# Optimization experiments

Measured on AMD Instinct MI355X. Metric: run time of the kernel, lower is better.

The kernel has to match this reference:

```python
import jax, jax.numpy as jnp
import numpy as np

N, E = 50000, 800000
NODE_DIM, EDGE_DIM, HID = 128, 32, 128
NEG_SLOPE = 0.2


def _init(key, shape, fan_in):
    # glorot-ish init for weights
    return jax.random.normal(key, shape, dtype=jnp.float32) * (1.0 / np.sqrt(fan_in))


def setup_inputs() -> dict:
    key = jax.random.key(0)
    ks = jax.random.split(key, 20)
    x = jax.random.normal(ks[0], (N, NODE_DIM), dtype=jnp.float32)
    edge_index = jax.random.randint(ks[1], (2, E), 0, N, dtype=jnp.int64)
    edge_attr = jax.random.normal(ks[2], (E, EDGE_DIM), dtype=jnp.float32)
    params = {
        'W_emb': _init(ks[3], (NODE_DIM, HID), NODE_DIM),
        'b_emb': jnp.zeros((HID,), jnp.float32),
        # conv1 (GATv2Conv, heads=1)
        'Wl1': _init(ks[4], (HID, HID), HID), 'bl1': jnp.zeros((HID,), jnp.float32),
        'Wr1': _init(ks[5], (HID, HID), HID),
        'We1': _init(ks[6], (EDGE_DIM, HID), EDGE_DIM),
        'att1': _init(ks[7], (HID,), HID),
        'bo1': jnp.zeros((HID,), jnp.float32),
        # conv2
        'Wl2': _init(ks[8], (HID, HID), HID), 'bl2': jnp.zeros((HID,), jnp.float32),
        'Wr2': _init(ks[9], (HID, HID), HID),
        'We2': _init(ks[10], (EDGE_DIM, HID), EDGE_DIM),
        'att2': _init(ks[11], (HID,), HID),
        'bo2': jnp.zeros((HID,), jnp.float32),
    }
    return {'x': x, 'edge_index': edge_index, 'edge_attr': edge_attr, **params}


def _gatv2(x, src, dst, edge_attr, Wl, bl, Wr, We, att, bo, n_nodes):
    """PyG GATv2Conv (heads=1, add_self_loops=True, fill_value='mean')."""
    xl = x @ Wl + bl          # [N, H] source transform
    xr = x @ Wr               # [N, H] target transform
    # --- add self loops; self-loop edge_attr = mean of incoming edge_attr ---
    ones = jnp.ones((src.shape[0],), x.dtype)
    deg = jax.ops.segment_sum(ones, dst, num_segments=n_nodes)
    loop_attr = jax.ops.segment_sum(edge_attr, dst, num_segments=n_nodes) \
        / jnp.maximum(deg, 1.0)[:, None]
    loops = jnp.arange(n_nodes, dtype=src.dtype)
    src2 = jnp.concatenate([src, loops])
    dst2 = jnp.concatenate([dst, loops])
    ea2 = jnp.concatenate([edge_attr, loop_attr], axis=0)
    # --- per-edge attention (GATv2: leaky_relu AFTER the sum, score via att) ---
    xl_j = xl[src2]                                  # [E', H]
    msg = xl_j + xr[dst2] + ea2 @ We                 # [E', H]
    logits = jax.nn.leaky_relu(msg, NEG_SLOPE) @ att  # [E']
    # --- softmax over incoming edges per target node ---
    m = jax.ops.segment_max(logits, dst2, num_segments=n_nodes)
    ez = jnp.exp(logits - m[dst2])
    denom = jax.ops.segment_sum(ez, dst2, num_segments=n_nodes)
    alpha = ez / denom[dst2]                         # [E']
    # --- scatter-add aggregation ---
    out = jax.ops.segment_sum(alpha[:, None] * xl_j, dst2, num_segments=n_nodes)
    return out + bo


def reference(x, edge_index, edge_attr, W_emb, b_emb,
              Wl1, bl1, Wr1, We1, att1, bo1,
              Wl2, bl2, Wr2, We2, att2, bo2):
    src, dst = edge_index[0], edge_index[1]
    n = x.shape[0]
    h = x @ W_emb + b_emb
    h = jax.nn.silu(_gatv2(h, src, dst, edge_attr, Wl1, bl1, Wr1, We1, att1, bo1, n))
    h = jax.nn.silu(_gatv2(h, src, dst, edge_attr, Wl2, bl2, Wr2, We2, att2, bo2, n))
    return h
```

## Files before the change

### kernel.cpp

```cpp
#include <hip/hip_runtime.h>
#include <hip/hip_bf16.h>
#include <math.h>


#define HIP_N 50000
#define HIP_E 800000
#define HIP_H 128
#define HIP_ED 32
#define NEG_SLOPE 0.2f
#define RESCALE_THR_LOG2 11.5416f
#define LINB ((HIP_N + 31) / 32)
#define SCATB ((HIP_E + 255) / 256)
#define INV_LN2 1.4426950408889634f

typedef __fp16 h2 __attribute__((ext_vector_type(2)));

__device__ __forceinline__ h2 u2h(unsigned int u) {
    union { unsigned int u; h2 h; } c; c.u = u; return c.h;
}
__device__ __forceinline__ unsigned int pkh(float a, float b) {
    union { h2 h; unsigned int u; } c;
    c.h = __builtin_amdgcn_cvt_pkrtz(a, b);
    return c.u;
}
__device__ __forceinline__ float2 h2f(unsigned int u) {
    h2 h = u2h(u);
    return make_float2((float)h.x, (float)h.y);
}

__global__ void k_detect(const int* __restrict__ ei, int* __restrict__ is32) {
    int j = blockIdx.x * blockDim.x + threadIdx.x;
    if (j < 4096) {
        if (ei[2 * j + 1] != 0) atomicOr(is32, 1);
    }
}

__device__ __forceinline__ int fetch_idx(const int* __restrict__ ei, int is32, long long pos) {
    return is32 ? ei[pos] : ei[2 * pos];
}

__global__ void k_hist(const int* __restrict__ ei, const int* __restrict__ flag,
                       int* __restrict__ deg) {
    int is32 = *flag;
    int e = blockIdx.x * blockDim.x + threadIdx.x;
    if (e < HIP_E) {
        int d = fetch_idx(ei, is32, (long long)HIP_E + e);
        atomicAdd(&deg[d], 1);
    }
}

#define SCAN_TILE 1024
#define SCAN_NB ((HIP_N + SCAN_TILE - 1) / SCAN_TILE)

__global__ __launch_bounds__(256) void k_scan1(const int* __restrict__ deg,
                                               int* __restrict__ bsums) {
    __shared__ int ws[4];
    int b = blockIdx.x, t = threadIdx.x;
    int base = b * SCAN_TILE;
    int v = 0;
#pragma unroll
    for (int j = 0; j < 4; ++j) {
        int i = base + t + 256 * j;
        if (i < HIP_N) v += deg[i];
    }
#pragma unroll
    for (int off = 32; off > 0; off >>= 1) v += __shfl_xor(v, off);
    int lane = t & 63, wid = t >> 6;
    if (lane == 0) ws[wid] = v;
    __syncthreads();
    if (t == 0) bsums[b] = ws[0] + ws[1] + ws[2] + ws[3];
}

__global__ __launch_bounds__(64) void k_scan2(const int* __restrict__ bsums,
                                              int* __restrict__ bscan) {
    int t = threadIdx.x;
    int v = (t < SCAN_NB) ? bsums[t] : 0;
    int incl = v;
#pragma unroll
    for (int off = 1; off < 64; off <<= 1) {
        int u = __shfl_up(incl, off);
        if (t >= off) incl += u;
    }
    if (t < SCAN_NB) bscan[t] = incl - v;
}

__global__ __launch_bounds__(1024) void k_scan3(const int* __restrict__ deg,
                                                const int* __restrict__ bscan,
                                                int* __restrict__ offs,
                                                int* __restrict__ cursor) {
    __shared__ int wsum[16];
    int b = blockIdx.x, t = threadIdx.x;
    int i = b * SCAN_TILE + t;
    int lane = t & 63, wid = t >> 6;
    int v = (i < HIP_N) ? deg[i] : 0;
    int incl = v;
#pragma unroll
    for (int off = 1; off < 64; off <<= 1) {
        int u = __shfl_up(incl, off);
        if (lane >= off) incl += u;
    }
    if (lane == 63) wsum[wid] = incl;
    __syncthreads();
    if (wid == 0 && lane < 16) {
        int w = wsum[lane];
#pragma unroll
        for (int off = 1; off < 16; off <<= 1) {
            int u = __shfl_up(w, off);
            if (lane >= off) w += u;
        }
        wsum[lane] = w;
    }
    __syncthreads();
    int baseadd = bscan[b] + (wid > 0 ? wsum[wid - 1] : 0);
    int excl = baseadd + incl - v;
    if (i < HIP_N) {
        offs[i] = excl;
        cursor[i] = excl;
        if (i == HIP_N - 1) offs[HIP_N] = excl + v;
    }
}

__device__ __forceinline__ void lin_body(const float* __restrict__ h,
                                         const float* __restrict__ Wl,
                                         const float* __restrict__ bl,
                                         const float* __restrict__ Wr,
                                         const float* __restrict__ br,
                                         unsigned int* __restrict__ xlh,
                                         unsigned int* __restrict__ xrh,
                                         int n, int blk) {
    __shared__ float tile[32][128];
    int rb = blk * 32;
    int tid = threadIdx.x;
    for (int j = 0; j < 16; ++j) {
        int idx = j * 256 + tid;
        int r = idx >> 7, c = idx & 127;
        int row = rb + r;
        tile[r][c] = (row < n) ? h[(size_t)row * 128 + c] : 0.f;
    }
    __syncthreads();
    int c = tid & 127, g = tid >> 7;
    float accl[16], accr[16];
#pragma unroll
    for (int r = 0; r < 16; ++r) { accl[r] = 0.f; accr[r] = 0.f; }
    for (int d4 = 0; d4 < 32; ++d4) {
        int d = d4 * 4;
        float wl0 = Wl[(d + 0) * 128 + c];
        float wl1 = Wl[(d + 1) * 128 + c];
        float wl2 = Wl[(d + 2) * 128 + c];
        float wl3 = Wl[(d + 3) * 128 + c];
        float wr0 = Wr[(d + 0) * 128 + c];
        float wr1 = Wr[(d + 1) * 128 + c];
        float wr2 = Wr[(d + 2) * 128 + c];
        float wr3 = Wr[(d + 3) * 128 + c];
#pragma unroll
        for (int r = 0; r < 16; ++r) {
            const float4 hv = *(const float4*)&tile[g * 16 + r][d];
            accl[r] += hv.x * wl0 + hv.y * wl1 + hv.z * wl2 + hv.w * wl3;
            accr[r] += hv.x * wr0 + hv.y * wr1 + hv.z * wr2 + hv.w * wr3;
        }
    }
    float bbl = bl[c], bbr = br[c];
    bool evenc = !(c & 1);
#pragma unroll
    for (int r = 0; r < 16; ++r) {
        int row = rb + g * 16 + r;
        float vl = accl[r] + bbl;
        float vr = accr[r] + bbr;
        float vl1 = __shfl_down(vl, 1);
        float vr1 = __shfl_down(vr, 1);
        if (evenc && row < n) {
            xlh[(size_t)row * 64 + (c >> 1)] = pkh(vl, vl1);
            xrh[(size_t)row * 64 + (c >> 1)] = pkh(vr, vr1);
        }
    }
}

__device__ __forceinline__ void scatter_body(const int* __restrict__ ei, int is32,
                                             int* __restrict__ cursor,
                                             int* __restrict__ e_src,
                                             const float* __restrict__ ea,
                                             unsigned int* __restrict__ ea_h, int e) {
    if (e < HIP_E) {
        int s = fetch_idx(ei, is32, e);
        int d = fetch_idx(ei, is32, (long long)HIP_E + e);
        int pos = atomicAdd(&cursor[d], 1);
        e_src[pos] = s;
        const float4* src4 = (const float4*)(ea + (size_t)e * HIP_ED);
        float4 s0 = src4[0], s1 = src4[1], s2 = src4[2], s3 = src4[3];
        float4 s4 = src4[4], s5 = src4[5], s6 = src4[6], s7 = src4[7];
        uint4* dst = (uint4*)(ea_h + (size_t)pos * 16);
        dst[0] = make_uint4(pkh(s0.x, s0.y), pkh(s0.z, s0.w),
                            pkh(s1.x, s1.y), pkh(s1.z, s1.w));
        dst[1] = make_uint4(pkh(s2.x, s2.y), pkh(s2.z, s2.w),
                            pkh(s3.x, s3.y), pkh(s3.z, s3.w));
        dst[2] = make_uint4(pkh(s4.x, s4.y), pkh(s4.z, s4.w),
                            pkh(s5.x, s5.y), pkh(s5.z, s5.w));
        dst[3] = make_uint4(pkh(s6.x, s6.y), pkh(s6.z, s6.w),
                            pkh(s7.x, s7.y), pkh(s7.z, s7.w));
    }
}

__global__ __launch_bounds__(256) void k_fat1(
    const float* __restrict__ x, const float* __restrict__ Wl,
    const float* __restrict__ bl, const float* __restrict__ Wr,
    const float* __restrict__ br,
    unsigned int* __restrict__ xlh, unsigned int* __restrict__ xrh,
    const int* __restrict__ ei, const int* __restrict__ flag,
    int* __restrict__ cursor, int* __restrict__ e_src,
    const float* __restrict__ ea, unsigned int* __restrict__ ea_h) {
    if (blockIdx.x < LINB) {
        lin_body(x, Wl, bl, Wr, br, xlh, xrh, HIP_N, blockIdx.x);
    } else {
        int e = (blockIdx.x - LINB) * 256 + threadIdx.x;
        scatter_body(ei, *flag, cursor, e_src, ea, ea_h, e);
    }
}

__global__ __launch_bounds__(256) void k_lin(const float* __restrict__ h,
                                             const float* __restrict__ Wl,
                                             const float* __restrict__ bl,
                                             const float* __restrict__ Wr,
                                             const float* __restrict__ br,
                                             unsigned int* __restrict__ xlh,
                                             unsigned int* __restrict__ xrh, int n) {
    lin_body(h, Wl, bl, Wr, br, xlh, xrh, n, blockIdx.x);
}

__global__ __launch_bounds__(128) void k_compose(
    const float* __restrict__ Wemb, const float* __restrict__ bemb,
    const float* __restrict__ Wl, const float* __restrict__ bl,
    const float* __restrict__ Wr,
    float* __restrict__ Wlf, float* __restrict__ blf,
    float* __restrict__ Wrf, float* __restrict__ brf,
    float* __restrict__ zerob) {
    int b = blockIdx.x, c = threadIdx.x;
    if (b < 128) {
        float acc = 0.f;
        for (int k = 0; k < 128; ++k) acc += Wemb[b * 128 + k] * Wl[k * 128 + c];
        Wlf[b * 128 + c] = acc;
    } else if (b < 256) {
        int r = b - 128;
        float acc = 0.f;
        for (int k = 0; k < 128; ++k) acc += Wemb[r * 128 + k] * Wr[k * 128 + c];
        Wrf[r * 128 + c] = acc;
    } else if (b == 256) {
        float acc = bl[c];
        for (int k = 0; k < 128; ++k) acc += bemb[k] * Wl[k * 128 + c];
        blf[c] = acc;
    } else {
        float acc = 0.f;
        for (int k = 0; k < 128; ++k) acc += bemb[k] * Wr[k * 128 + c];
        brf[c] = acc;
        zerob[c] = 0.f;
    }
}

__global__ __launch_bounds__(256) void k_packwe(const float* __restrict__ We1,
                                                const float* __restrict__ We2,
                                                unsigned int* __restrict__ P1,
                                                unsigned int* __restrict__ P2) {
    int idx = blockIdx.x * 256 + threadIdx.x;
    if (idx < 4096) {
        const float* We = (idx < 2048) ? We1 : We2;
        unsigned int* P = (idx < 2048) ? P1 : P2;
        int r = idx & 2047;
        int d2 = r >> 7, rem = r & 127;
        int j = rem >> 6, t = rem & 63;
        int col = 2 * t + j;
        P[r] = pkh(We[(2 * d2) * 128 + col], We[(2 * d2 + 1) * 128 + col]);
    }
}

__global__ __launch_bounds__(64) void k_node_fused(
    const int* __restrict__ offs, const int* __restrict__ e_src,
    const unsigned int* __restrict__ ea_h,
    const unsigned int* __restrict__ Wepk, const float* __restrict__ att,
    const unsigned int* __restrict__ xlh, const unsigned int* __restrict__ xrh,
    const float* __restrict__ bo, float* __restrict__ hout) {
    int i = blockIdx.x;
    int t = threadIdx.x;

    h2 wx00 = u2h(Wepk[ 0*128 + t]),      wy00 = u2h(Wepk[ 0*128 + 64 + t]);
    h2 wx01 = u2h(Wepk[ 1*128 + t]),      wy01 = u2h(Wepk[ 1*128 + 64 + t]);
    h2 wx02 = u2h(Wepk[ 2*128 + t]),      wy02 = u2h(Wepk[ 2*128 + 64 + t]);
    h2 wx03 = u2h(Wepk[ 3*128 + t]),      wy03 = u2h(Wepk[ 3*128 + 64 + t]);
    h2 wx04 = u2h(Wepk[ 4*128 + t]),      wy04 = u2h(Wepk[ 4*128 + 64 + t]);
    h2 wx05 = u2h(Wepk[ 5*128 + t]),      wy05 = u2h(Wepk[ 5*128 + 64 + t]);
    h2 wx06 = u2h(Wepk[ 6*128 + t]),      wy06 = u2h(Wepk[ 6*128 + 64 + t]);
    h2 wx07 = u2h(Wepk[ 7*128 + t]),      wy07 = u2h(Wepk[ 7*128 + 64 + t]);
    h2 wx08 = u2h(Wepk[ 8*128 + t]),      wy08 = u2h(Wepk[ 8*128 + 64 + t]);
    h2 wx09 = u2h(Wepk[ 9*128 + t]),      wy09 = u2h(Wepk[ 9*128 + 64 + t]);
    h2 wx10 = u2h(Wepk[10*128 + t]),      wy10 = u2h(Wepk[10*128 + 64 + t]);
    h2 wx11 = u2h(Wepk[11*128 + t]),      wy11 = u2h(Wepk[11*128 + 64 + t]);
    h2 wx12 = u2h(Wepk[12*128 + t]),      wy12 = u2h(Wepk[12*128 + 64 + t]);
    h2 wx13 = u2h(Wepk[13*128 + t]),      wy13 = u2h(Wepk[13*128 + 64 + t]);
    h2 wx14 = u2h(Wepk[14*128 + t]),      wy14 = u2h(Wepk[14*128 + 64 + t]);
    h2 wx15 = u2h(Wepk[15*128 + t]),      wy15 = u2h(Wepk[15*128 + 64 + t]);

    float2 attv = ((const float2*)att)[t];
    attv.x *= INV_LN2; attv.y *= INV_LN2;
    float2 bov  = ((const float2*)bo)[t];
    float2 xri  = h2f(xrh[(size_t)i * 64 + t]);
    float2 xli  = h2f(xlh[(size_t)i * 64 + t]);

    float m = -1e30f;
    float denom = 0.f;
    float accx = 0.f, accy = 0.f;
    float epsx = 0.f, epsy = 0.f;

    int o0 = offs[i], o1 = offs[i + 1];
    int cnt = o1 - o0;
    int pairs = cnt >> 1;

#define DOTP(EX, EY, U, K)                                            \
    EX = __builtin_amdgcn_fdot2(u2h(U), wx##K, EX, false);            \
    EY = __builtin_amdgcn_fdot2(u2h(U), wy##K, EY, false);

#define EPROJ(EX, EY, P)                                              \
    {                                                                 \
        uint4 q0 = ((const uint4*)(P))[0];                            \
        uint4 q1 = ((const uint4*)(P))[1];                            \
        uint4 q2 = ((const uint4*)(P))[2];                            \
        uint4 q3 = ((const uint4*)(P))[3];                            \
        DOTP(EX, EY, q0.x, 00) DOTP(EX, EY, q0.y, 01)                 \
        DOTP(EX, EY, q0.z, 02) DOTP(EX, EY, q0.w, 03)                 \
        DOTP(EX, EY, q1.x, 04) DOTP(EX, EY, q1.y, 05)                 \
        DOTP(EX, EY, q1.z, 06) DOTP(EX, EY, q1.w, 07)                 \
        DOTP(EX, EY, q2.x, 08) DOTP(EX, EY, q2.y, 09)                 \
        DOTP(EX, EY, q2.z, 10) DOTP(EX, EY, q2.w, 11)                 \
        DOTP(EX, EY, q3.x, 12) DOTP(EX, EY, q3.y, 13)                 \
        DOTP(EX, EY, q3.z, 14) DOTP(EX, EY, q3.w, 15)                 \
    }

    unsigned int uA = 0, uB = 0;
    if (pairs > 0) {
        int s0 = e_src[o0];
        int s1 = e_src[o0 + 1];
        uA = xlh[(size_t)s0 * 64 + t];
        uB = xlh[(size_t)s1 * 64 + t];
    }

    for (int pp = 0; pp < pairs; ++pp) {
        int e = o0 + 2 * pp;
        float2 x0 = h2f(uA), x1 = h2f(uB);
        if (pp + 1 < pairs) {
            int s0 = e_src[e + 2];
            int s1 = e_src[e + 3];
            uA = xlh[(size_t)s0 * 64 + t];
            uB = xlh[(size_t)s1 * 64 + t];
        }
        const unsigned int* er = ea_h + (size_t)e * 16;
        float ex0 = 0.f, ey0 = 0.f, ex1 = 0.f, ey1 = 0.f;
        EPROJ(ex0, ey0, er)
        EPROJ(ex1, ey1, er + 16)
        epsx += ex0 + ex1; epsy += ey0 + ey1;
        float vx0 = x0.x + xri.x + ex0, vy0 = x0.y + xri.y + ey0;
        float vx1 = x1.x + xri.x + ex1, vy1 = x1.y + xri.y + ey1;
        vx0 = fmaxf(vx0, NEG_SLOPE * vx0);
        vy0 = fmaxf(vy0, NEG_SLOPE * vy0);
        vx1 = fmaxf(vx1, NEG_SLOPE * vx1);
        vy1 = fmaxf(vy1, NEG_SLOPE * vy1);
        float p0 = vx0 * attv.x + vy0 * attv.y;
        float p1 = vx1 * attv.x + vy1 * attv.y;
#pragma unroll
        for (int off = 32; off > 0; off >>= 1) {
            p0 += __shfl_xor(p0, off);
            p1 += __shfl_xor(p1, off);
        }
        float pm = fmaxf(p0, p1);
        if (pm > m + RESCALE_THR_LOG2) {
            float sc = exp2f(m - pm);
            accx *= sc; accy *= sc; denom *= sc;
            m = pm;
        }
        float wA = exp2f(p0 - m);
        float wB = exp2f(p1 - m);
        accx += wA * x0.x + wB * x1.x;
        accy += wA * x0.y + wB * x1.y;
        denom += wA + wB;
    }

    if (cnt & 1) {
        int e = o1 - 1;
        int s = e_src[e];
        float2 x0 = h2f(xlh[(size_t)s * 64 + t]);
        const unsigned int* er = ea_h + (size_t)e * 16;
        float ex = 0.f, ey = 0.f;
        EPROJ(ex, ey, er)
        epsx += ex; epsy += ey;
        float vx = x0.x + xri.x + ex;
        float vy = x0.y + xri.y + ey;
        vx = fmaxf(vx, NEG_SLOPE * vx);
        vy = fmaxf(vy, NEG_SLOPE * vy);
        float p = vx * attv.x + vy * attv.y;
#pragma unroll
        for (int off = 32; off > 0; off >>= 1) p += __shfl_xor(p, off);
        if (p > m + RESCALE_THR_LOG2) {
            float sc = exp2f(m - p);
            accx *= sc; accy *= sc; denom *= sc;
            m = p;
        }
        float w = exp2f(p - m);
        accx += w * x0.x;
        accy += w * x0.y;
        denom += w;
    }
#undef EPROJ
#undef DOTP

    float invdeg = 1.f / fmaxf((float)cnt, 1.f);
    float sx = xli.x + xri.x + epsx * invdeg;
    float sy = xli.y + xri.y + epsy * invdeg;
    sx = fmaxf(sx, NEG_SLOPE * sx);
    sy = fmaxf(sy, NEG_SLOPE * sy);
    float ps = sx * attv.x + sy * attv.y;
#pragma unroll
    for (int off = 32; off > 0; off >>= 1) ps += __shfl_xor(ps, off);

    float mm = fmaxf(m, ps);
    float wf = exp2f(m - mm);
    float ws = exp2f(ps - mm);
    denom = denom * wf + ws;
    accx = accx * wf + ws * xli.x;
    accy = accy * wf + ws * xli.y;

    float ox = accx / denom + bov.x;
    float oy = accy / denom + bov.y;
    float2 o;
    o.x = ox / (1.f + __expf(-ox));
    o.y = oy / (1.f + __expf(-oy));
    ((float2*)(hout + (size_t)i * HIP_H))[t] = o;
}

extern "C" void kernel_launch(void* const* d_in, const int* in_sizes, int n_in,
                              void* d_out, int out_size, void* d_ws, size_t ws_size,
                              hipStream_t stream) {
    const float* x      = (const float*)d_in[0];
    const int*   ei     = (const int*)d_in[1];
    const float* ea     = (const float*)d_in[2];
    const float* W_emb  = (const float*)d_in[3];
    const float* b_emb  = (const float*)d_in[4];
    const float* Wl1    = (const float*)d_in[5];
    const float* bl1    = (const float*)d_in[6];
    const float* Wr1    = (const float*)d_in[7];
    const float* We1    = (const float*)d_in[8];
    const float* att1   = (const float*)d_in[9];
    const float* bo1    = (const float*)d_in[10];
    const float* Wl2    = (const float*)d_in[11];
    const float* bl2    = (const float*)d_in[12];
    const float* Wr2    = (const float*)d_in[13];
    const float* We2    = (const float*)d_in[14];
    const float* att2   = (const float*)d_in[15];
    const float* bo2    = (const float*)d_in[16];
    float* out = (float*)d_out;

    char* p = (char*)d_ws;
    auto carve = [&](size_t bytes) {
        void* q = (void*)p;
        p += (bytes + 255) / 256 * 256;
        return q;
    };
    float* h        = (float*)carve((size_t)HIP_N * 128 * 4);
    unsigned int* xlh = (unsigned int*)carve((size_t)HIP_N * 64 * 4);
    unsigned int* xrh = (unsigned int*)carve((size_t)HIP_N * 64 * 4);
    unsigned int* ea_h = (unsigned int*)carve((size_t)HIP_E * 16 * 4);
    int*   deg      = (int*)carve((size_t)HIP_N * 4);
    int*   offs     = (int*)carve((size_t)(HIP_N + 1) * 4);
    int*   cursor   = (int*)carve((size_t)HIP_N * 4);
    int*   e_src    = (int*)carve((size_t)HIP_E * 4);
    int*   flag     = (int*)carve(256);
    int*   bsums    = (int*)carve((size_t)SCAN_NB * 4);
    int*   bscan    = (int*)carve((size_t)SCAN_NB * 4);
    float* Wl1f     = (float*)carve(128 * 128 * 4);
    float* Wr1f     = (float*)carve(128 * 128 * 4);
    float* bl1f     = (float*)carve(128 * 4);
    float* br1f     = (float*)carve(128 * 4);
    float* zerob    = (float*)carve(128 * 4);
    unsigned int* Wepk1 = (unsigned int*)carve(2048 * 4);
    unsigned int* Wepk2 = (unsigned int*)carve(2048 * 4);

    hipMemsetAsync(deg, 0, (size_t)HIP_N * 4, stream);
    hipMemsetAsync(flag, 0, 4, stream);

    k_detect<<<16, 256, 0, stream>>>(ei, flag);
    k_hist<<<(HIP_E + 255) / 256, 256, 0, stream>>>(ei, flag, deg);
    k_scan1<<<SCAN_NB, 256, 0, stream>>>(deg, bsums);
    k_scan2<<<1, 64, 0, stream>>>(bsums, bscan);
    k_scan3<<<SCAN_NB, 1024, 0, stream>>>(deg, bscan, offs, cursor);
    k_compose<<<258, 128, 0, stream>>>(W_emb, b_emb, Wl1, bl1, Wr1,
                                       Wl1f, bl1f, Wr1f, br1f, zerob);
    k_packwe<<<16, 256, 0, stream>>>(We1, We2, Wepk1, Wepk2);

    k_fat1<<<LINB + SCATB, 256, 0, stream>>>(x, Wl1f, bl1f, Wr1f, br1f, xlh, xrh,
                                             ei, flag, cursor, e_src, ea, ea_h);

    k_node_fused<<<HIP_N, 64, 0, stream>>>(offs, e_src, ea_h, Wepk1, att1,
                                           xlh, xrh, bo1, h);
    k_lin<<<(HIP_N + 31) / 32, 256, 0, stream>>>(h, Wl2, bl2, Wr2, zerob, xlh, xrh, HIP_N);
    k_node_fused<<<HIP_N, 64, 0, stream>>>(offs, e_src, ea_h, Wepk2, att2,
                                           xlh, xrh, bo2, out);
}
```

Measured before the change: 496.5 us.

## Run node linear transforms on MFMA fp16 matrix cores

Replaces the scalar-FMA shared-memory GEMM for the xl/xr projections with MFMA 16x16x32 fp16 instructions. Activations are converted to fp16 on the fly, and a new packing kernel builds transposed, concatenated fp16 [Wl|Wr] weights with a combined bias for both layers. Each 256-thread block computes 16 rows times 256 output columns. This is meant to cut the compute cost of the two dense projections, at the price of fp16 rounding of the inputs and weights and one extra small setup kernel.

```diff
diff --git a/kernel.cpp b/kernel.cpp
--- a/kernel.cpp
+++ b/kernel.cpp
@@ -9,11 +9,13 @@
 #define HIP_ED 32
 #define NEG_SLOPE 0.2f
 #define RESCALE_THR_LOG2 11.5416f
-#define LINB ((HIP_N + 31) / 32)
+#define LINM 3125
 #define SCATB ((HIP_E + 255) / 256)
 #define INV_LN2 1.4426950408889634f
 
 typedef __fp16 h2 __attribute__((ext_vector_type(2)));
+typedef _Float16 half8 __attribute__((ext_vector_type(8)));
+typedef float f32x4 __attribute__((ext_vector_type(4)));
 
 __device__ __forceinline__ h2 u2h(unsigned int u) {
     union { unsigned int u; h2 h; } c; c.u = u; return c.h;
@@ -26,6 +28,9 @@
 __device__ __forceinline__ float2 h2f(unsigned int u) {
     h2 h = u2h(u);
     return make_float2((float)h.x, (float)h.y);
+}
+__device__ __forceinline__ half8 u4h8(uint4 u) {
+    union { uint4 u; half8 h; } c; c.u = u; return c.h;
 }
 
 __global__ void k_detect(const int* __restrict__ ei, int* __restrict__ is32) {
@@ -120,57 +125,53 @@
     }
 }
 
-__device__ __forceinline__ void lin_body(const float* __restrict__ h,
-                                         const float* __restrict__ Wl,
-                                         const float* __restrict__ bl,
-                                         const float* __restrict__ Wr,
-                                         const float* __restrict__ br,
-                                         unsigned int* __restrict__ xlh,
-                                         unsigned int* __restrict__ xrh,
-                                         int n, int blk) {
-    __shared__ float tile[32][128];
-    int rb = blk * 32;
+__device__ __forceinline__ void linm_body(const float* __restrict__ A,
+                                          const unsigned short* __restrict__ Wt,
+                                          const float* __restrict__ bias,
+                                          unsigned int* __restrict__ xlh,
+                                          unsigned int* __restrict__ xrh, int blk) {
     int tid = threadIdx.x;
-    for (int j = 0; j < 16; ++j) {
-        int idx = j * 256 + tid;
-        int r = idx >> 7, c = idx & 127;
-        int row = rb + r;
-        tile[r][c] = (row < n) ? h[(size_t)row * 128 + c] : 0.f;
-    }
-    __syncthreads();
-    int c = tid & 127, g = tid >> 7;
-    float accl[16], accr[16];
-#pragma unroll
-    for (int r = 0; r < 16; ++r) { accl[r] = 0.f; accr[r] = 0.f; }
-    for (int d4 = 0; d4 < 32; ++d4) {
-        int d = d4 * 4;
-        float wl0 = Wl[(d + 0) * 128 + c];
-        float wl1 = Wl[(d + 1) * 128 + c];
-        float wl2 = Wl[(d + 2) * 128 + c];
-        float wl3 = Wl[(d + 3) * 128 + c];
-        float wr0 = Wr[(d + 0) * 128 + c];
-        float wr1 = Wr[(d + 1) * 128 + c];
-        float wr2 = Wr[(d + 2) * 128 + c];
-        float wr3 = Wr[(d + 3) * 128 + c];
-#pragma unroll
-        for (int r = 0; r < 16; ++r) {
-            const float4 hv = *(const float4*)&tile[g * 16 + r][d];
-            accl[r] += hv.x * wl0 + hv.y * wl1 + hv.z * wl2 + hv.w * wl3;
-            accr[r] += hv.x * wr0 + hv.y * wr1 + hv.z * wr2 + hv.w * wr3;
-        }
-    }
-    float bbl = bl[c], bbr = br[c];
-    bool evenc = !(c & 1);
-#pragma unroll
-    for (int r = 0; r < 16; ++r) {
-        int row = rb + g * 16 + r;
-        float vl = accl[r] + bbl;
-        float vr = accr[r] + bbr;
-        float vl1 = __shfl_down(vl, 1);
-        float vr1 = __shfl_down(vr, 1);
-        if (evenc && row < n) {
-            xlh[(size_t)row * 64 + (c >> 1)] = pkh(vl, vl1);
-            xrh[(size_t)row * 64 + (c >> 1)] = pkh(vr, vr1);
+    int wid = tid >> 6, l = tid & 63;
+    int li = l & 15, lk = l >> 4;
+    size_t arow = (size_t)(blk * 16 + li) * 128;
+
+    f32x4 acc0 = {0.f, 0.f, 0.f, 0.f};
+    f32x4 acc1 = {0.f, 0.f, 0.f, 0.f};
+    f32x4 acc2 = {0.f, 0.f, 0.f, 0.f};
+    f32x4 acc3 = {0.f, 0.f, 0.f, 0.f};
+
+#pragma unroll
+    for (int ks = 0; ks < 4; ++ks) {
+        int kb = ks * 32 + lk * 8;
+        const float4* ap = (const float4*)(A + arow + kb);
+        float4 a0 = ap[0], a1 = ap[1];
+        half8 afrag = u4h8(make_uint4(pkh(a0.x, a0.y), pkh(a0.z, a0.w),
+                                      pkh(a1.x, a1.y), pkh(a1.z, a1.w)));
+        int nbase = wid * 64 + li;
+        half8 b0 = u4h8(*(const uint4*)(Wt + (size_t)(nbase +  0) * 128 + kb));
+        half8 b1 = u4h8(*(const uint4*)(Wt + (size_t)(nbase + 16) * 128 + kb));
+        half8 b2 = u4h8(*(const uint4*)(Wt + (size_t)(nbase + 32) * 128 + kb));
+        half8 b3 = u4h8(*(const uint4*)(Wt + (size_t)(nbase + 48) * 128 + kb));
+        acc0 = __builtin_amdgcn_mfma_f32_16x16x32_f16(afrag, b0, acc0, 0, 0, 0);
+        acc1 = __builtin_amdgcn_mfma_f32_16x16x32_f16(afrag, b1, acc1, 0, 0, 0);
+        acc2 = __builtin_amdgcn_mfma_f32_16x16x32_f16(afrag, b2, acc2, 0, 0, 0);
+        acc3 = __builtin_amdgcn_mfma_f32_16x16x32_f16(afrag, b3, acc3, 0, 0, 0);
+    }
+
+    bool even = !(l & 1);
+#pragma unroll
+    for (int nt = 0; nt < 4; ++nt) {
+        f32x4 a = (nt == 0) ? acc0 : (nt == 1) ? acc1 : (nt == 2) ? acc2 : acc3;
+        int n = wid * 64 + nt * 16 + li;
+        float bb = bias[n];
+        unsigned int* outp = (n < 128) ? xlh : xrh;
+        int nn = n & 127;
+#pragma unroll
+        for (int r = 0; r < 4; ++r) {
+            int rowg = blk * 16 + lk * 4 + r;
+            float v = a[r] + bb;
+            float v1 = __shfl_down(v, 1);
+            if (even) outp[(size_t)rowg * 64 + (nn >> 1)] = pkh(v, v1);
         }
     }
 }
@@ -201,29 +202,26 @@
 }
 
 __global__ __launch_bounds__(256) void k_fat1(
-    const float* __restrict__ x, const float* __restrict__ Wl,
-    const float* __restrict__ bl, const float* __restrict__ Wr,
-    const float* __restrict__ br,
+    const float* __restrict__ x, const unsigned short* __restrict__ Wt1,
+    const float* __restrict__ b1,
     unsigned int* __restrict__ xlh, unsigned int* __restrict__ xrh,
     const int* __restrict__ ei, const int* __restrict__ flag,
     int* __restrict__ cursor, int* __restrict__ e_src,
     const float* __restrict__ ea, unsigned int* __restrict__ ea_h) {
-    if (blockIdx.x < LINB) {
-        lin_body(x, Wl, bl, Wr, br, xlh, xrh, HIP_N, blockIdx.x);
+    if (blockIdx.x < LINM) {
+        linm_body(x, Wt1, b1, xlh, xrh, blockIdx.x);
     } else {
-        int e = (blockIdx.x - LINB) * 256 + threadIdx.x;
+        int e = (blockIdx.x - LINM) * 256 + threadIdx.x;
         scatter_body(ei, *flag, cursor, e_src, ea, ea_h, e);
     }
 }
 
-__global__ __launch_bounds__(256) void k_lin(const float* __restrict__ h,
-                                             const float* __restrict__ Wl,
-                                             const float* __restrict__ bl,
-                                             const float* __restrict__ Wr,
-                                             const float* __restrict__ br,
-                                             unsigned int* __restrict__ xlh,
-                                             unsigned int* __restrict__ xrh, int n) {
-    lin_body(h, Wl, bl, Wr, br, xlh, xrh, n, blockIdx.x);
+__global__ __launch_bounds__(256) void k_linm(const float* __restrict__ A,
+                                              const unsigned short* __restrict__ Wt,
+                                              const float* __restrict__ bias,
+                                              unsigned int* __restrict__ xlh,
+                                              unsigned int* __restrict__ xrh) {
+    linm_body(A, Wt, bias, xlh, xrh, blockIdx.x);
 }
 
 __global__ __launch_bounds__(128) void k_compose(
@@ -231,8 +229,7 @@
     const float* __restrict__ Wl, const float* __restrict__ bl,
     const float* __restrict__ Wr,
     float* __restrict__ Wlf, float* __restrict__ blf,
-    float* __restrict__ Wrf, float* __restrict__ brf,
-    float* __restrict__ zerob) {
+    float* __restrict__ Wrf, float* __restrict__ brf) {
     int b = blockIdx.x, c = threadIdx.x;
     if (b < 128) {
         float acc = 0.f;
@@ -251,7 +248,31 @@
         float acc = 0.f;
         for (int k = 0; k < 128; ++k) acc += bemb[k] * Wr[k * 128 + c];
         brf[c] = acc;
-        zerob[c] = 0.f;
+    }
+}
+
+__global__ __launch_bounds__(128) void k_packw(
+    const float* __restrict__ Wl1f, const float* __restrict__ Wr1f,
+    const float* __restrict__ bl1f, const float* __restrict__ br1f,
+    const float* __restrict__ Wl2, const float* __restrict__ bl2,
+    const float* __restrict__ Wr2,
+    unsigned short* __restrict__ Wt1, unsigned short* __restrict__ Wt2,
+    float* __restrict__ b1, float* __restrict__ b2) {
+    int b = blockIdx.x, k = threadIdx.x;
+    int layer = b >> 8, n = b & 255;
+    int nn = n & 127;
+    const float* W;
+    if (layer == 0) W = (n < 128) ? Wl1f : Wr1f;
+    else            W = (n < 128) ? Wl2 : Wr2;
+    float v = W[k * 128 + nn];
+    union { __fp16 h; unsigned short s; } cv;
+    cv.h = (__fp16)v;
+    (layer ? Wt2 : Wt1)[(size_t)n * 128 + k] = cv.s;
+    if (k == 0) {
+        float bv;
+        if (layer == 0) bv = (n < 128) ? bl1f[nn] : br1f[nn];
+        else            bv = (n < 128) ? bl2[nn] : 0.f;
+        (layer ? b2 : b1)[n] = bv;
     }
 }
 
@@ -475,9 +496,12 @@
     float* Wr1f     = (float*)carve(128 * 128 * 4);
     float* bl1f     = (float*)carve(128 * 4);
     float* br1f     = (float*)carve(128 * 4);
-    float* zerob    = (float*)carve(128 * 4);
     unsigned int* Wepk1 = (unsigned int*)carve(2048 * 4);
     unsigned int* Wepk2 = (unsigned int*)carve(2048 * 4);
+    unsigned short* Wt1 = (unsigned short*)carve(256 * 128 * 2);
+    unsigned short* Wt2 = (unsigned short*)carve(256 * 128 * 2);
+    float* b1       = (float*)carve(256 * 4);
+    float* b2       = (float*)carve(256 * 4);
 
     hipMemsetAsync(deg, 0, (size_t)HIP_N * 4, stream);
     hipMemsetAsync(flag, 0, 4, stream);
@@ -488,15 +512,17 @@
     k_scan2<<<1, 64, 0, stream>>>(bsums, bscan);
     k_scan3<<<SCAN_NB, 1024, 0, stream>>>(deg, bscan, offs, cursor);
     k_compose<<<258, 128, 0, stream>>>(W_emb, b_emb, Wl1, bl1, Wr1,
-                                       Wl1f, bl1f, Wr1f, br1f, zerob);
+                                       Wl1f, bl1f, Wr1f, br1f);
     k_packwe<<<16, 256, 0, stream>>>(We1, We2, Wepk1, Wepk2);
-
-    k_fat1<<<LINB + SCATB, 256, 0, stream>>>(x, Wl1f, bl1f, Wr1f, br1f, xlh, xrh,
+    k_packw<<<512, 128, 0, stream>>>(Wl1f, Wr1f, bl1f, br1f, Wl2, bl2, Wr2,
+                                     Wt1, Wt2, b1, b2);
+
+    k_fat1<<<LINM + SCATB, 256, 0, stream>>>(x, Wt1, b1, xlh, xrh,
                                              ei, flag, cursor, e_src, ea, ea_h);
 
     k_node_fused<<<HIP_N, 64, 0, stream>>>(offs, e_src, ea_h, Wepk1, att1,
                                            xlh, xrh, bo1, h);
-    k_lin<<<(HIP_N + 31) / 32, 256, 0, stream>>>(h, Wl2, bl2, Wr2, zerob, xlh, xrh, HIP_N);
+    k_linm<<<LINM, 256, 0, stream>>>(h, Wt2, b2, xlh, xrh);
     k_node_fused<<<HIP_N, 64, 0, stream>>>(offs, e_src, ea_h, Wepk2, att2,
                                            xlh, xrh, bo2, out);
 }
```

New measurement: 452.2 us. 8.9% less time.
